# Optimization experiments

Hardware: AMD Instinct MI355X
Metric: run time of the kernel (lower is better)

## Reference

```python
import jax, jax.numpy as jnp
import numpy as np
from math import sqrt

MIN_SCORE = 0.05
MAX_OVERLAP = 0.45
TOP_K = 200


def make_priors():
    feature_dims = {'mid': 18, 'end': 9, 'a': 9, 'b': 5, 'c': 3, 'd': 1}
    obj_scales = {'mid': 0.2, 'end': 0.2, 'a': 0.375, 'b': 0.55, 'c': 0.725, 'd': 0.9}
    aspect_ratio = {'mid': [1.0, 2.0, 3.0, 0.5, 0.333], 'end': [1.0, 2.0, 3.0, 0.5, 0.333],
                    'a': [1.0, 2.0, 3.0, 0.5, 0.333], 'b': [1.0, 2.0, 3.0, 0.5, 0.333],
                    'c': [1.0, 2.0, 0.5], 'd': [1.0, 2.0, 0.5]}
    fmaps = list(feature_dims.keys())
    boxes = []
    for k, fmap in enumerate(fmaps):
        for i in range(feature_dims[fmap]):
            for j in range(feature_dims[fmap]):
                cx = (j + 0.5) / feature_dims[fmap]
                cy = (i + 0.5) / feature_dims[fmap]
                for ratio in aspect_ratio[fmap]:
                    boxes.append([cx, cy, obj_scales[fmap] * sqrt(ratio), obj_scales[fmap] / sqrt(ratio)])
                if fmap in ['mid', 'end', 'a', 'b', 'c']:
                    s = sqrt(obj_scales[fmap] * obj_scales[fmaps[k + 1]])
                else:
                    s = 1.0
                boxes.append([cx, cy, s, s])
    return np.clip(np.asarray(boxes, dtype=np.float32), 0.0, 1.0)  # [3106, 4]


def setup_inputs() -> dict:
    key = jax.random.key(0)
    k1, k2 = jax.random.split(key)
    return {
        'predicted_locs': jax.random.normal(k1, (4, 3106, 4), dtype=jnp.float32),
        'predicted_scores': jax.random.normal(k2, (4, 3106, 21), dtype=jnp.float32),
        'priors_cxcy': jnp.asarray(make_priors()),
    }


def _decode(predicted_locs, priors):
    # gcxgcy_to_cxcy then cxcy_to_xy (standard SSD variances 0.1 / 0.2)
    cxcy = predicted_locs[..., :2] * priors[..., 2:] / 10.0 + priors[..., :2]
    wh = jnp.exp(predicted_locs[..., 2:] / 5.0) * priors[..., 2:]
    return jnp.concatenate([cxcy - wh / 2.0, cxcy + wh / 2.0], axis=-1)  # xyxy


def _detect_image(boxes_i, probs_i):
    # boxes_i: [P,4] xyxy, probs_i: [P,C] softmax scores
    P = boxes_i.shape[0]
    C = probs_i.shape[1]
    # full pairwise Jaccard overlap [P,P]
    lt = jnp.maximum(boxes_i[:, None, :2], boxes_i[None, :, :2])
    rb = jnp.minimum(boxes_i[:, None, 2:], boxes_i[None, :, 2:])
    inter = jnp.prod(jnp.clip(rb - lt, 0.0), axis=-1)
    area = jnp.prod(boxes_i[:, 2:] - boxes_i[:, :2], axis=-1)
    iou = inter / (area[:, None] + area[None, :] - inter)

    cls = probs_i[:, 1:].T                      # [C-1, P], skip background
    valid = cls > MIN_SCORE
    order = jnp.argsort(-jnp.where(valid, cls, -jnp.inf), axis=1)  # [C-1, P]
    valid_s = jnp.take_along_axis(valid, order, axis=1)
    iou_sg = jax.lax.stop_gradient(iou)

    def body(i, suppress):                       # greedy NMS over sorted boxes, all classes at once
        bi = order[:, i]                         # [C-1] prior index per class
        rows = jnp.take_along_axis(iou_sg[bi], order, axis=1) > MAX_OVERLAP  # [C-1, P]
        skip = suppress[:, i] | ~valid_s[:, i]
        proc = (suppress | rows).at[:, i].set(False)
        return jnp.where(skip[:, None], suppress, proc)

    suppress = jax.lax.fori_loop(0, P, body, ~valid_s)
    keep = ~suppress                             # [C-1, P] (sorted order)

    scores_s = jnp.take_along_axis(cls, order, axis=1)
    cand_scores = jnp.where(keep, scores_s, -jnp.inf).reshape(-1)     # [(C-1)*P]
    cand_boxes = boxes_i[order].reshape(-1, 4)
    cand_labels = jnp.broadcast_to(jnp.arange(1, C, dtype=jnp.int32)[:, None], (C - 1, P)).reshape(-1)

    top_scores, top_idx = jax.lax.top_k(cand_scores, TOP_K)
    top_boxes = cand_boxes[top_idx]
    top_labels = cand_labels[top_idx]

    has = jnp.isfinite(top_scores)
    top_scores = jnp.where(has, top_scores, 0.0)
    top_boxes = jnp.where(has[:, None], top_boxes, 0.0)
    top_labels = jnp.where(has, top_labels, 0)
    count = jnp.minimum(jnp.sum(keep).astype(jnp.int32), TOP_K)

    # torch fallback: a single background box when nothing is detected
    none = count == 0
    top_boxes = top_boxes.at[0].set(jnp.where(none, jnp.array([0.0, 0.0, 1.0, 1.0], dtype=top_boxes.dtype), top_boxes[0]))
    count = jnp.where(none, jnp.int32(1), count)
    return top_boxes, top_labels, top_scores, count


def reference(predicted_locs, predicted_scores, priors_cxcy):
    probs = jax.nn.softmax(predicted_scores, axis=2)          # [B,P,C]
    boxes = _decode(predicted_locs, priors_cxcy[None])        # [B,P,4]
    all_boxes, all_labels, all_scores, counts = jax.vmap(_detect_image)(boxes, probs)
    return all_boxes, all_labels, all_scores, counts
```

## Files before the change

### kernel.cpp

```cpp
#include <hip/hip_runtime.h>

#define NB 4
#define NPRI 3106
#define NC 21
#define NCLS 20
#define KMAX 200
#define NMAX 1024
#define WMAX 16
#define TMAX (WMAX*(WMAX+1)/2)
#define MIN_SC 0.05f
#define MAX_OV 0.45f

#define F_PROBS 0
#define F_KEYS  (F_PROBS + NB*NCLS*NPRI)
#define F_BOXES (F_KEYS + NB*NCLS*NMAX*2)
#define F_AREAS (F_BOXES + NB*NCLS*NMAX*4)
#define F_NCAND (F_AREAS + NB*NCLS*NMAX)
#define F_M     (F_NCAND + 128)
#define F_POOL  (F_M + NB*NCLS*WMAX*NMAX*2)
#define F_CNT   (F_POOL + NB*NCLS*KMAX*2)
#define F_DONE  (F_CNT + NB*NCLS)

#define OUT_BOXES  0
#define OUT_LABELS (NB*KMAX*4)
#define OUT_SCORES (OUT_LABELS + NB*KMAX)
#define OUT_COUNTS (OUT_SCORES + NB*KMAX)

__device__ __forceinline__ float bcast(float v, int l) {
    return __uint_as_float(__builtin_amdgcn_readlane(__float_as_uint(v), l));
}

__device__ __forceinline__ void decode_box(const float* __restrict__ locs,
                                           const float* __restrict__ priors,
                                           int b, int pi,
                                           float& x1, float& y1, float& x2, float& y2) {
    const float* l  = locs + ((size_t)b * NPRI + pi) * 4;
    const float* pr = priors + (size_t)pi * 4;
    float pcx = pr[0], pcy = pr[1], pw = pr[2], ph = pr[3];
    float cx = l[0] * pw / 10.0f + pcx;
    float cy = l[1] * ph / 10.0f + pcy;
    float w  = expf(l[2] / 5.0f) * pw;
    float h  = expf(l[3] / 5.0f) * ph;
    x1 = cx - w / 2.0f;  y1 = cy - h / 2.0f;
    x2 = cx + w / 2.0f;  y2 = cy + h / 2.0f;
}

__device__ __forceinline__ unsigned long long shfl_xor_u64(unsigned long long v, int m) {
    unsigned lo = (unsigned)v, hi = (unsigned)(v >> 32);
    lo = __shfl_xor(lo, m);
    hi = __shfl_xor(hi, m);
    return ((unsigned long long)hi << 32) | lo;
}

__device__ __forceinline__ void softmax_push(const float* __restrict__ v, int c,
                                             int r, unsigned long long* keys,
                                             int* n_sh) {
    float m = -1e30f;
    #pragma unroll
    for (int k = 0; k < NC; ++k) m = fmaxf(m, v[k]);
    float sum = 0.0f, ec = 0.0f;
    #pragma unroll
    for (int k = 0; k < NC; ++k) {
        float e = expf(v[k] - m);
        sum += e;
        if (k == c + 1) ec = e;
    }
    float val = ec / sum;
    if (val > MIN_SC) {
        int idx = atomicAdd(n_sh, 1);
        if (idx < NMAX) {
            unsigned int sb = __float_as_uint(val);
            keys[idx] = ((unsigned long long)(~sb) << 32) | (unsigned int)r;
        }
    }
}

__global__ __launch_bounds__(1024)
void det_prep(const float* __restrict__ scores, const float* __restrict__ locs,
              const float* __restrict__ priors, float* __restrict__ ws) {
    const int bc  = blockIdx.x;
    const int b   = bc / NCLS;
    const int c   = bc - b * NCLS;
    const int tid = threadIdx.x;

    __shared__ unsigned long long keys[NMAX];
    __shared__ int n_sh;
    if (tid == 0) n_sh = 0;
    __syncthreads();

    const float* sbase = scores + (size_t)b * NPRI * NC;
    {
        float v0[NC], v1[NC], v2[NC];
        const float* s0 = sbase + (size_t)(tid)        * NC;
        const float* s1 = sbase + (size_t)(tid + 1024) * NC;
        const float* s2 = sbase + (size_t)(tid + 2048) * NC;
        #pragma unroll
        for (int k = 0; k < NC; ++k) { v0[k] = s0[k]; }
        #pragma unroll
        for (int k = 0; k < NC; ++k) { v1[k] = s1[k]; }
        #pragma unroll
        for (int k = 0; k < NC; ++k) { v2[k] = s2[k]; }
        softmax_push(v0, c, tid,        keys, &n_sh);
        softmax_push(v1, c, tid + 1024, keys, &n_sh);
        softmax_push(v2, c, tid + 2048, keys, &n_sh);
        if (tid < NPRI - 3072) {
            float v3[NC];
            const float* s3 = sbase + (size_t)(tid + 3072) * NC;
            #pragma unroll
            for (int k = 0; k < NC; ++k) { v3[k] = s3[k]; }
            softmax_push(v3, c, tid + 3072, keys, &n_sh);
        }
    }
    __syncthreads();
    int n = n_sh; if (n > NMAX) n = NMAX;

    unsigned long long mykey = (tid < n) ? keys[tid] : ~0ull;
    __syncthreads();
    for (int k = 2; k <= NMAX; k <<= 1) {
        for (int j = k >> 1; j > 0; j >>= 1) {
            unsigned long long other;
            if (j >= 64) {
                keys[tid] = mykey;
                __syncthreads();
                other = keys[tid ^ j];
                __syncthreads();
            } else {
                other = shfl_xor_u64(mykey, j);
            }
            bool lower    = (tid & j) == 0;
            bool up       = (tid & k) == 0;
            bool take_min = (lower == up);
            bool swap     = take_min ? (other < mykey) : (other > mykey);
            mykey = swap ? other : mykey;
        }
    }

    if (tid == 0) ((int*)(ws + F_NCAND))[bc] = n;
    unsigned long long* gk = (unsigned long long*)(ws + F_KEYS) + (size_t)bc * NMAX;
    float4* gb = (float4*)(ws + F_BOXES) + (size_t)bc * NMAX;
    float*  ga = ws + F_AREAS + (size_t)bc * NMAX;
    if (tid < n) {
        gk[tid] = mykey;
        int pi = (int)(mykey & 0xFFFFFFFFull);
        float x1, y1, x2, y2;
        decode_box(locs, priors, b, pi, x1, y1, x2, y2);
        gb[tid] = make_float4(x1, y1, x2, y2);
        ga[tid] = (x2 - x1) * (y2 - y1);
    }
}

__global__ __launch_bounds__(256)
void det_mbuild(float* __restrict__ ws) {
    if (blockIdx.x == 0 && blockIdx.y == 0 && threadIdx.x < NB)
        ((int*)(ws + F_DONE))[threadIdx.x] = 0;

    const int bc = blockIdx.y;
    const int t  = blockIdx.x * 4 + (threadIdx.x >> 6);
    if (t >= TMAX) return;
    const int lane = threadIdx.x & 63;
    int tj = 0;
    while ((tj + 1) * (tj + 2) / 2 <= t) ++tj;
    const int w = t - tj * (tj + 1) / 2;
    const int n = ((const int*)(ws + F_NCAND))[bc];
    const int bi0 = w * 64, bj0 = tj * 64;
    if (bj0 >= n) return;

    const float4* bx = (const float4*)(ws + F_BOXES) + (size_t)bc * NMAX;
    const float*  ar = ws + F_AREAS + (size_t)bc * NMAX;
    const float4 bi = bx[bi0 + lane];
    const float  ai = ar[bi0 + lane];
    const float4 bj = bx[bj0 + lane];
    const float  aj = ar[bj0 + lane];
    const unsigned long long vm =
        (n - bi0 >= 64) ? ~0ull : ((1ull << (n - bi0)) - 1ull);
    const bool diag = (w == tj);
    unsigned long long myword = 0ull;

    #pragma unroll
    for (int jj = 0; jj < 64; jj += 2) {
        float ax1 = bcast(bj.x, jj),     ay1 = bcast(bj.y, jj);
        float ax2 = bcast(bj.z, jj),     ay2 = bcast(bj.w, jj);
        float aau = bcast(aj, jj);
        float bx1 = bcast(bj.x, jj + 1), by1 = bcast(bj.y, jj + 1);
        float bx2 = bcast(bj.z, jj + 1), by2 = bcast(bj.w, jj + 1);
        float bau = bcast(aj, jj + 1);

        float alx = fmaxf(bi.x, ax1), aly = fmaxf(bi.y, ay1);
        float arx = fminf(bi.z, ax2), ary = fminf(bi.w, ay2);
        float blx = fmaxf(bi.x, bx1), bly = fmaxf(bi.y, by1);
        float brx = fminf(bi.z, bx2), bry = fminf(bi.w, by2);
        float adx = fmaxf(arx - alx, 0.0f), ady = fmaxf(ary - aly, 0.0f);
        float bdx = fmaxf(brx - blx, 0.0f), bdy = fmaxf(bry - bly, 0.0f);
        float ain = adx * ady;
        float bin = bdx * bdy;
        float au  = ai + aau - ain;
        float bu  = ai + bau - bin;
        float at  = MAX_OV * au;
        float bt  = MAX_OV * bu;
        bool akeep = ain > at;
        bool bkeep = bin > bt;
        bool anear = fabsf(ain - at) <= at * 6e-7f;
        bool bnear = fabsf(bin - bt) <= bt * 6e-7f;
        if (__ballot(anear || bnear)) {
            float aio = ain / au;
            float bio = bin / bu;
            akeep = anear ? (aio > MAX_OV) : akeep;
            bkeep = bnear ? (bio > MAX_OV) : bkeep;
        }
        unsigned long long abits = __ballot(akeep) & vm;
        unsigned long long bbits = __ballot(bkeep) & vm;
        if (diag) {
            abits &= (1ull << jj) - 1ull;
            bbits &= (1ull << (jj + 1)) - 1ull;
        }
        if (lane == jj)     myword = abits;
        if (lane == jj + 1) myword = bbits;
    }
    if (bj0 + lane < n)
        ((unsigned long long*)(ws + F_M))
            [((size_t)bc * WMAX + w) * NMAX + bj0 + lane] = myword;
}

__global__ __launch_bounds__(256)
void det_finishA(float* __restrict__ ws, float* __restrict__ out) {
    const int bc   = blockIdx.x;
    const int b    = bc / NCLS;
    const int c    = bc - b * NCLS;
    const int cls  = c + 1;
    const int tid  = threadIdx.x;

    if (tid < 64) {
        const int lane = tid;
        const int n    = ((const int*)(ws + F_NCAND))[bc];
        const unsigned long long* Mb =
            (const unsigned long long*)(ws + F_M) + (size_t)bc * WMAX * NMAX;

        unsigned long long kw[WMAX];
        #pragma unroll
        for (int w = 0; w < WMAX; ++w) kw[w] = 0ull;

        const unsigned long long lmask = (1ull << lane) - 1ull;
        #pragma unroll
        for (int w = 0; w < WMAX; ++w) {
            if (w * 64 < n) {
                int cc = w * 64 + lane;
                bool valid = cc < n;
                unsigned long long pre = 0ull;
                #pragma unroll
                for (int v = 0; v < WMAX; ++v)
                    if (v < w) pre |= Mb[(size_t)v * NMAX + cc] & kw[v];
                unsigned long long dg = Mb[(size_t)w * NMAX + cc] & lmask;
                bool sup0 = (pre != 0ull);
                unsigned long long K = __ballot(valid && !sup0);
                for (int it = 0; it < 64; ++it) {
                    bool sup = sup0 || ((dg & K) != 0ull);
                    unsigned long long Kn = __ballot(valid && !sup);
                    if (Kn == K) break;
                    K = Kn;
                }
                kw[w] = K;
            }
        }

        int pref[WMAX + 1];
        pref[0] = 0;
        #pragma unroll
        for (int w = 0; w < WMAX; ++w) pref[w + 1] = pref[w] + __popcll(kw[w]);
        if (lane == 0) ((int*)(ws + F_CNT))[bc] = pref[WMAX];

        const unsigned long long* gk =
            (const unsigned long long*)(ws + F_KEYS) + (size_t)bc * NMAX;
        unsigned long long* pool =
            (unsigned long long*)(ws + F_POOL) + (size_t)bc * KMAX;
        const unsigned long long ctag = (unsigned long long)(cls << 12);
        #pragma unroll
        for (int w = 0; w < WMAX; ++w) {
            unsigned long long kwv = kw[w];
            int cc = w * 64 + lane;
            if (cc < n && ((kwv >> lane) & 1ull)) {
                int pos = pref[w] + __popcll(kwv & lmask);
                if (pos < KMAX) pool[pos] = gk[cc] | ctag;
            }
        }
    }

    {
        int idx = c * 256 + tid;
        if (idx < KMAX * 4) {
            out[OUT_BOXES + (size_t)b * KMAX * 4 + idx] = 0.0f;
        } else if (idx < KMAX * 4 + KMAX) {
            out[OUT_LABELS + b * KMAX + (idx - KMAX * 4)] = 0.0f;
        } else if (idx < KMAX * 4 + 2 * KMAX) {
            out[OUT_SCORES + b * KMAX + (idx - KMAX * 4 - KMAX)] = 0.0f;
        }
    }
}

__global__ __launch_bounds__(256)
void det_finishB(const float* __restrict__ locs, const float* __restrict__ priors,
                 const float* __restrict__ ws, float* __restrict__ out) {
    const int bc   = blockIdx.x;
    const int b    = bc / NCLS;
    const int c    = bc - b * NCLS;
    const int tid  = threadIdx.x;

    __shared__ unsigned long long lpool[NCLS * KMAX];
    __shared__ int cnts[NCLS];

    const int* cnt = (const int*)(ws + F_CNT);
    if (tid < NCLS) cnts[tid] = cnt[b * NCLS + tid];
    __syncthreads();

    const unsigned long long* pool =
        (const unsigned long long*)(ws + F_POOL) + (size_t)b * NCLS * KMAX;
    for (int i = tid; i < NCLS * KMAX; i += 256) {
        int c2 = i / KMAX, r = i - c2 * KMAX;
        int mc2 = cnts[c2] < KMAX ? cnts[c2] : KMAX;
        lpool[i] = (r < mc2) ? pool[i] : ~0ull;
    }
    __syncthreads();

    if (c == 0 && tid == 0) {
        int tot = 0;
        for (int c2 = 0; c2 < NCLS; ++c2) tot += cnts[c2];
        int count = tot < KMAX ? tot : KMAX;
        if (tot == 0) {
            float* ob = out + OUT_BOXES + (size_t)b * KMAX * 4;
            ob[0] = 0.0f; ob[1] = 0.0f; ob[2] = 1.0f; ob[3] = 1.0f;
            count = 1;
        }
        out[OUT_COUNTS + b] = (float)count;
    }

    const int mc = cnts[c] < KMAX ? cnts[c] : KMAX;
    if (tid < mc) {
        unsigned long long key = lpool[c * KMAX + tid];
        int rank = 0;
        #pragma unroll
        for (int c2 = 0; c2 < NCLS; ++c2) {
            int lo = 0, hi = KMAX;
            #pragma unroll
            for (int s = 0; s < 8; ++s) {
                int mid = (lo + hi) >> 1;
                int midc = mid < KMAX ? mid : KMAX - 1;
                unsigned long long v = lpool[c2 * KMAX + midc];
                bool lt = (lo < hi) && (v < key);
                lo = lt ? mid + 1 : lo;
                hi = lt ? hi : mid;
            }
            rank += lo;
        }
        if (rank < KMAX) {
            unsigned int lo32 = (unsigned int)key;
            int pi  = lo32 & 0xFFF;
            int lab = (lo32 >> 12) & 0x1F;
            float sc = __uint_as_float(~(unsigned int)(key >> 32));
            float x1, y1, x2, y2;
            decode_box(locs, priors, b, pi, x1, y1, x2, y2);
            float* ob = out + OUT_BOXES + ((size_t)b * KMAX + rank) * 4;
            ob[0] = x1; ob[1] = y1; ob[2] = x2; ob[3] = y2;
            out[OUT_LABELS + b * KMAX + rank] = (float)lab;
            out[OUT_SCORES + b * KMAX + rank] = sc;
        }
    }
}

extern "C" void kernel_launch(void* const* d_in, const int* in_sizes, int n_in,
                              void* d_out, int out_size, void* d_ws, size_t ws_size,
                              hipStream_t stream) {
    const float* locs   = (const float*)d_in[0];
    const float* scores = (const float*)d_in[1];
    const float* priors = (const float*)d_in[2];
    float* out = (float*)d_out;
    float* ws  = (float*)d_ws;

    det_prep<<<NB * NCLS, 1024, 0, stream>>>(scores, locs, priors, ws);
    det_mbuild<<<dim3((TMAX + 3) / 4, NB * NCLS), 256, 0, stream>>>(ws);
    det_finishA<<<NB * NCLS, 256, 0, stream>>>(ws, out);
    det_finishB<<<NB * NCLS, 256, 0, stream>>>(locs, priors, ws, out);
}
```

Before: 149.4 us.

## Split softmax/compaction into a grid-wide kernel separate from per-class sort

The old 80-block prep kernel, where each block computed softmax over all 3106 priors for a single class, is replaced by three kernels. A zero kernel clears the counters, a fully parallel kernel runs one thread per (image, prior, class) and compacts candidates into global memory with global atomics, and a per-class sort kernel loads those keys and bitonic-sorts them. The aim is to fill the whole GPU for the softmax stage instead of only 80 blocks. In exchange it adds two kernel launches, global atomics and a global-memory round trip, and it recomputes the full softmax for each class, so total arithmetic rises.

```diff
diff --git a/kernel.cpp b/kernel.cpp
--- a/kernel.cpp
+++ b/kernel.cpp
@@ -12,6 +12,7 @@
 #define MAX_OV 0.45f
 
 #define F_PROBS 0
+#define F_UKEYS F_PROBS
 #define F_KEYS  (F_PROBS + NB*NCLS*NPRI)
 #define F_BOXES (F_KEYS + NB*NCLS*NMAX*2)
 #define F_AREAS (F_BOXES + NB*NCLS*NMAX*4)
@@ -52,70 +53,60 @@
     return ((unsigned long long)hi << 32) | lo;
 }
 
-__device__ __forceinline__ void softmax_push(const float* __restrict__ v, int c,
-                                             int r, unsigned long long* keys,
-                                             int* n_sh) {
+__global__ __launch_bounds__(128)
+void det_zero(float* __restrict__ ws) {
+    ((int*)(ws + F_NCAND))[threadIdx.x] = 0;
+}
+
+__global__ __launch_bounds__(256)
+void det_softmax_compact(const float* __restrict__ scores, float* __restrict__ ws) {
+    const int t = blockIdx.x * 256 + threadIdx.x;
+    if (t >= NB * NPRI * NCLS) return;
+    const int b   = t / (NPRI * NCLS);
+    const int rem = t - b * (NPRI * NCLS);
+    const int p   = rem / NCLS;
+    const int c   = rem - p * NCLS;
+
+    const float* s = scores + ((size_t)b * NPRI + p) * NC;
     float m = -1e30f;
     #pragma unroll
-    for (int k = 0; k < NC; ++k) m = fmaxf(m, v[k]);
+    for (int k = 0; k < NC; ++k) m = fmaxf(m, s[k]);
     float sum = 0.0f, ec = 0.0f;
     #pragma unroll
     for (int k = 0; k < NC; ++k) {
-        float e = expf(v[k] - m);
+        float e = expf(s[k] - m);
         sum += e;
         if (k == c + 1) ec = e;
     }
     float val = ec / sum;
     if (val > MIN_SC) {
-        int idx = atomicAdd(n_sh, 1);
+        const int bc = b * NCLS + c;
+        int idx = atomicAdd((int*)(ws + F_NCAND) + bc, 1);
         if (idx < NMAX) {
             unsigned int sb = __float_as_uint(val);
-            keys[idx] = ((unsigned long long)(~sb) << 32) | (unsigned int)r;
+            ((unsigned long long*)(ws + F_UKEYS))[(size_t)bc * NMAX + idx] =
+                ((unsigned long long)(~sb) << 32) | (unsigned int)p;
         }
     }
 }
 
 __global__ __launch_bounds__(1024)
-void det_prep(const float* __restrict__ scores, const float* __restrict__ locs,
-              const float* __restrict__ priors, float* __restrict__ ws) {
+void det_sort(const float* __restrict__ locs, const float* __restrict__ priors,
+              float* __restrict__ ws) {
     const int bc  = blockIdx.x;
     const int b   = bc / NCLS;
-    const int c   = bc - b * NCLS;
     const int tid = threadIdx.x;
 
     __shared__ unsigned long long keys[NMAX];
-    __shared__ int n_sh;
-    if (tid == 0) n_sh = 0;
-    __syncthreads();
-
-    const float* sbase = scores + (size_t)b * NPRI * NC;
-    {
-        float v0[NC], v1[NC], v2[NC];
-        const float* s0 = sbase + (size_t)(tid)        * NC;
-        const float* s1 = sbase + (size_t)(tid + 1024) * NC;
-        const float* s2 = sbase + (size_t)(tid + 2048) * NC;
-        #pragma unroll
-        for (int k = 0; k < NC; ++k) { v0[k] = s0[k]; }
-        #pragma unroll
-        for (int k = 0; k < NC; ++k) { v1[k] = s1[k]; }
-        #pragma unroll
-        for (int k = 0; k < NC; ++k) { v2[k] = s2[k]; }
-        softmax_push(v0, c, tid,        keys, &n_sh);
-        softmax_push(v1, c, tid + 1024, keys, &n_sh);
-        softmax_push(v2, c, tid + 2048, keys, &n_sh);
-        if (tid < NPRI - 3072) {
-            float v3[NC];
-            const float* s3 = sbase + (size_t)(tid + 3072) * NC;
-            #pragma unroll
-            for (int k = 0; k < NC; ++k) { v3[k] = s3[k]; }
-            softmax_push(v3, c, tid + 3072, keys, &n_sh);
-        }
-    }
-    __syncthreads();
-    int n = n_sh; if (n > NMAX) n = NMAX;
-
-    unsigned long long mykey = (tid < n) ? keys[tid] : ~0ull;
-    __syncthreads();
+
+    int* ncand = (int*)(ws + F_NCAND);
+    int n = ncand[bc]; if (n > NMAX) n = NMAX;
+    if (tid == 0) ncand[bc] = n;
+
+    const unsigned long long* uk =
+        (const unsigned long long*)(ws + F_UKEYS) + (size_t)bc * NMAX;
+    unsigned long long mykey = (tid < n) ? uk[tid] : ~0ull;
+
     for (int k = 2; k <= NMAX; k <<= 1) {
         for (int j = k >> 1; j > 0; j >>= 1) {
             unsigned long long other;
@@ -135,7 +126,6 @@
         }
     }
 
-    if (tid == 0) ((int*)(ws + F_NCAND))[bc] = n;
     unsigned long long* gk = (unsigned long long*)(ws + F_KEYS) + (size_t)bc * NMAX;
     float4* gb = (float4*)(ws + F_BOXES) + (size_t)bc * NMAX;
     float*  ga = ws + F_AREAS + (size_t)bc * NMAX;
@@ -374,7 +364,10 @@
     float* out = (float*)d_out;
     float* ws  = (float*)d_ws;
 
-    det_prep<<<NB * NCLS, 1024, 0, stream>>>(scores, locs, priors, ws);
+    det_zero<<<1, 128, 0, stream>>>(ws);
+    const int ntot = NB * NPRI * NCLS;
+    det_softmax_compact<<<(ntot + 255) / 256, 256, 0, stream>>>(scores, ws);
+    det_sort<<<NB * NCLS, 1024, 0, stream>>>(locs, priors, ws);
     det_mbuild<<<dim3((TMAX + 3) / 4, NB * NCLS), 256, 0, stream>>>(ws);
     det_finishA<<<NB * NCLS, 256, 0, stream>>>(ws, out);
     det_finishB<<<NB * NCLS, 256, 0, stream>>>(locs, priors, ws, out);
```

New measurement: 238.8 us. +59.9%, slower.
